# Performance work log

Measured on AMD Instinct MI355X. Metric: run time of the kernel, lower is better.

## Reference

```python
import jax, jax.numpy as jnp
import numpy as np

N_NODES = 100000
N_EDGES = 1600000
IN_DIM = 256
OUT_DIM = 128


def setup_inputs() -> dict:
    key = jax.random.key(0)
    ks = jax.random.split(key, 8)
    x = jax.random.normal(ks[0], (N_NODES, IN_DIM), dtype=jnp.float32)
    # glorot-ish init scaling
    W = jax.random.normal(ks[1], (IN_DIM, OUT_DIM), dtype=jnp.float32) * (6.0 / (IN_DIM + OUT_DIM)) ** 0.5
    fsW = jax.random.normal(ks[2], (IN_DIM, OUT_DIM), dtype=jnp.float32) * (6.0 / (IN_DIM + OUT_DIM)) ** 0.5
    f_weights = jax.random.normal(ks[3], (2 * OUT_DIM, 1), dtype=jnp.float32) * (6.0 / (2 * OUT_DIM + 1)) ** 0.5
    f_bias = jnp.zeros((1,), dtype=jnp.float32)
    # degrees in [1, 64], strictly positive so pow(deg, -p) is finite
    dia_adj = jax.random.uniform(ks[4], (N_NODES,), dtype=jnp.float32) * 63.0 + 1.0
    row = jax.random.randint(ks[5], (N_EDGES,), 0, N_NODES, dtype=jnp.int32)
    col = jax.random.randint(ks[6], (N_EDGES,), 0, N_NODES, dtype=jnp.int32)
    return {"x": x, "W": W, "fsW": fsW, "f_weights": f_weights,
            "f_bias": f_bias, "dia_adj": dia_adj, "row": row, "col": col}


def reference(x, W, fsW, f_weights, f_bias, dia_adj, row, col):
    # pre_sup = x @ weights_, fpre_sup = x @ fs_weights  (dropout=0, dense inputs)
    pre_sup = x @ W                 # [N, out]
    fpre_sup = x @ fsW              # [N, out]
    d = W.shape[1]
    # concat([vi, vj]) @ f_weights == vi @ f_weights[:d] + vj @ f_weights[d:]
    wi, wj = f_weights[:d], f_weights[d:]
    score = jax.nn.sigmoid(fpre_sup[row] @ wi + fpre_sup[col] @ wj + f_bias)  # [E, 1]
    # degree-power normalization: (deg_i * deg_j) ** (-sigmoid_score)
    deg_vivj = (dia_adj[row] * dia_adj[col])[:, None]                         # [E, 1]
    vals = jnp.power(deg_vivj, -score)[:, 0]                                  # [E]
    # sparse matmul: out[r] += vals_e * pre_sup[c] for each edge e=(r,c)
    msg = vals[:, None] * pre_sup[col]                                        # [E, out]
    out = jax.ops.segment_sum(msg, row, num_segments=x.shape[0])              # [N, out]
    return jax.nn.relu(out)
```

## Files before the change

kernel.cpp:

```cpp
#include <hip/hip_runtime.h>

#define N_NODES 100000
#define N_EDGES 1600000
#define IN_DIM 256
#define OUT_DIM 128
#define BROWS 100
#define NBK 1000
#define PBLK 128
#define EPB 12500

typedef __attribute__((ext_vector_type(4))) float f32x4;
typedef __attribute__((ext_vector_type(8))) short s16x8;

__device__ inline unsigned short f2bf(float f) {
    union { float f; unsigned int u; } a; a.f = f;
    unsigned int r = a.u + 0x7fffu + ((a.u >> 16) & 1u);
    return (unsigned short)(r >> 16);
}
__device__ inline float bf2f(unsigned short h) {
    union { unsigned int u; float f; } a; a.u = ((unsigned int)h) << 16;
    return a.f;
}

__global__ __launch_bounds__(256) void kprep(
        const float* __restrict__ fsW, const float* __restrict__ fw,
        const float* __restrict__ W, const int* __restrict__ row,
        float* __restrict__ u, float* __restrict__ v,
        unsigned short* __restrict__ wt, int* __restrict__ hist_t) {
    __shared__ int h[NBK];
    __shared__ float wi[128], wj[128];
    const int t = threadIdx.x, blk = blockIdx.x;
    if (blk < PBLK) {
        wt[blk * 256 + t] = f2bf(W[(size_t)t * 128 + blk]);
        for (int b = t; b < NBK; b += 256) h[b] = 0;
        __syncthreads();
        const int e0 = blk * EPB;
        for (int i = t; i < EPB; i += 256)
            atomicAdd(&h[row[e0 + i] / BROWS], 1);
        __syncthreads();
        for (int b = t; b < NBK; b += 256)
            hist_t[b * PBLK + blk] = h[b];
    } else {
        if (t < 128) wi[t] = fw[t]; else wj[t - 128] = fw[t];
        __syncthreads();
        const float* rowp = fsW + (size_t)t * OUT_DIM;
        float su = 0.f, sv = 0.f;
        for (int d = 0; d < 128; d += 4) {
            float4 a = *(const float4*)(rowp + d);
            su += a.x * wi[d] + a.y * wi[d + 1] + a.z * wi[d + 2] + a.w * wi[d + 3];
            sv += a.x * wj[d] + a.y * wj[d + 1] + a.z * wj[d + 2] + a.w * wj[d + 3];
        }
        u[t] = su; v[t] = sv;
    }
}

__global__ __launch_bounds__(256) void gemm_mfma(
        const float* __restrict__ x, const unsigned short* __restrict__ wt,
        const float* __restrict__ u, const float* __restrict__ v,
        unsigned short* __restrict__ psb, float* __restrict__ si, float* __restrict__ sj) {
    __shared__ unsigned short xa[64 * 136];

    const int t = threadIdx.x;
    const int wave = t >> 6, lane = t & 63;
    const int l15 = lane & 15, lhi = lane >> 4;
    const int row = t >> 2, quad = t & 3;
    const int brow = blockIdx.x * 64;
    const int gnode = brow + row;
    const bool fullblk = (brow + 64 <= N_NODES);
    const bool valid = gnode < N_NODES;

    f32x4 acc[4][2];
#pragma unroll
    for (int mi = 0; mi < 4; ++mi)
#pragma unroll
        for (int ni = 0; ni < 2; ++ni) acc[mi][ni] = (f32x4){0.f, 0.f, 0.f, 0.f};
    float su = 0.f, sv = 0.f;

#pragma unroll
    for (int ph = 0; ph < 2; ++ph) {
        const float* xp = x + (size_t)gnode * IN_DIM + ph * 128 + quad * 32;
        const float* up = u + ph * 128 + quad * 32;
        const float* vp = v + ph * 128 + quad * 32;
        if (fullblk) {
#pragma unroll
            for (int cc = 0; cc < 4; ++cc) {
                float4 a0 = ((const float4*)xp)[cc * 2];
                float4 a1 = ((const float4*)xp)[cc * 2 + 1];
                float4 u0 = ((const float4*)up)[cc * 2], u1 = ((const float4*)up)[cc * 2 + 1];
                float4 v0 = ((const float4*)vp)[cc * 2], v1 = ((const float4*)vp)[cc * 2 + 1];
                su = fmaf(a0.x, u0.x, su); su = fmaf(a0.y, u0.y, su);
                su = fmaf(a0.z, u0.z, su); su = fmaf(a0.w, u0.w, su);
                su = fmaf(a1.x, u1.x, su); su = fmaf(a1.y, u1.y, su);
                su = fmaf(a1.z, u1.z, su); su = fmaf(a1.w, u1.w, su);
                sv = fmaf(a0.x, v0.x, sv); sv = fmaf(a0.y, v0.y, sv);
                sv = fmaf(a0.z, v0.z, sv); sv = fmaf(a0.w, v0.w, sv);
                sv = fmaf(a1.x, v1.x, sv); sv = fmaf(a1.y, v1.y, sv);
                sv = fmaf(a1.z, v1.z, sv); sv = fmaf(a1.w, v1.w, sv);
                union { unsigned short h[8]; uint4 q; } pk;
                pk.h[0] = f2bf(a0.x); pk.h[1] = f2bf(a0.y); pk.h[2] = f2bf(a0.z); pk.h[3] = f2bf(a0.w);
                pk.h[4] = f2bf(a1.x); pk.h[5] = f2bf(a1.y); pk.h[6] = f2bf(a1.z); pk.h[7] = f2bf(a1.w);
                *(uint4*)&xa[row * 136 + quad * 32 + cc * 8] = pk.q;
            }
        } else {
#pragma unroll
            for (int cc = 0; cc < 4; ++cc) {
                float4 a0 = make_float4(0.f, 0.f, 0.f, 0.f), a1 = a0;
                if (valid) {
                    a0 = ((const float4*)xp)[cc * 2];
                    a1 = ((const float4*)xp)[cc * 2 + 1];
                    float4 u0 = ((const float4*)up)[cc * 2], u1 = ((const float4*)up)[cc * 2 + 1];
                    float4 v0 = ((const float4*)vp)[cc * 2], v1 = ((const float4*)vp)[cc * 2 + 1];
                    su = fmaf(a0.x, u0.x, su); su = fmaf(a0.y, u0.y, su);
                    su = fmaf(a0.z, u0.z, su); su = fmaf(a0.w, u0.w, su);
                    su = fmaf(a1.x, u1.x, su); su = fmaf(a1.y, u1.y, su);
                    su = fmaf(a1.z, u1.z, su); su = fmaf(a1.w, u1.w, su);
                    sv = fmaf(a0.x, v0.x, sv); sv = fmaf(a0.y, v0.y, sv);
                    sv = fmaf(a0.z, v0.z, sv); sv = fmaf(a0.w, v0.w, sv);
                    sv = fmaf(a1.x, v1.x, sv); sv = fmaf(a1.y, v1.y, sv);
                    sv = fmaf(a1.z, v1.z, sv); sv = fmaf(a1.w, v1.w, sv);
                }
                union { unsigned short h[8]; uint4 q; } pk;
                pk.h[0] = f2bf(a0.x); pk.h[1] = f2bf(a0.y); pk.h[2] = f2bf(a0.z); pk.h[3] = f2bf(a0.w);
                pk.h[4] = f2bf(a1.x); pk.h[5] = f2bf(a1.y); pk.h[6] = f2bf(a1.z); pk.h[7] = f2bf(a1.w);
                *(uint4*)&xa[row * 136 + quad * 32 + cc * 8] = pk.q;
            }
        }
        __syncthreads();

        {
            const unsigned short* wb0 = wt + (size_t)(wave * 32 + l15) * IN_DIM + ph * 128 + lhi * 8;
            s16x8 bfr[4][2];
#pragma unroll
            for (int ks = 0; ks < 4; ++ks) {
                bfr[ks][0] = *(const s16x8*)(wb0 + ks * 32);
                bfr[ks][1] = *(const s16x8*)(wb0 + (size_t)16 * IN_DIM + ks * 32);
            }
#pragma unroll
            for (int ks = 0; ks < 4; ++ks) {
                const int k0 = ks * 32 + lhi * 8;
                s16x8 afr[4];
#pragma unroll
                for (int mi = 0; mi < 4; ++mi)
                    afr[mi] = *(const s16x8*)&xa[(mi * 16 + l15) * 136 + k0];
#pragma unroll
                for (int mi = 0; mi < 4; ++mi)
#pragma unroll
                    for (int ni = 0; ni < 2; ++ni)
                        acc[mi][ni] = __builtin_amdgcn_mfma_f32_16x16x32_bf16(
                            afr[mi], bfr[ks][ni], acc[mi][ni], 0, 0, 0);
            }
        }
        __syncthreads();
    }

    su += __shfl_xor(su, 1); su += __shfl_xor(su, 2);
    sv += __shfl_xor(sv, 1); sv += __shfl_xor(sv, 2);
    if (quad == 0 && valid) { si[gnode] = su; sj[gnode] = sv; }

    unsigned short* cl = xa;
#pragma unroll
    for (int mi = 0; mi < 4; ++mi)
#pragma unroll
        for (int ni = 0; ni < 2; ++ni) {
            const int colb = wave * 32 + ni * 16 + l15;
#pragma unroll
            for (int j = 0; j < 4; ++j)
                cl[(mi * 16 + lhi * 4 + j) * 128 + colb] = f2bf(acc[mi][ni][j]);
        }
    __syncthreads();
    {
        const int rl = t >> 2;
        const int cb = (t & 3) * 32;
        if (brow + rl < N_NODES) {
            const uint4* src = (const uint4*)&cl[rl * 128 + cb];
            uint4* dst = (uint4*)&psb[(size_t)(brow + rl) * OUT_DIM + cb];
            dst[0] = src[0]; dst[1] = src[1]; dst[2] = src[2]; dst[3] = src[3];
        }
    }
}

__global__ __launch_bounds__(1024) void kbscan(const int* __restrict__ hist_t,
                                               int* __restrict__ bpre) {
    __shared__ int s[1024];
    const int t = threadIdx.x;
    int v = 0;
    if (t < NBK) {
        const int* hp = hist_t + t * PBLK;
        for (int k = 0; k < PBLK; ++k) v += hp[k];
    }
    s[t] = v;
    __syncthreads();
    for (int off = 1; off < 1024; off <<= 1) {
        int nv = (t >= off) ? s[t - off] : 0;
        __syncthreads();
        s[t] += nv;
        __syncthreads();
    }
    if (t < NBK) bpre[t] = s[t] - v;
    if (t == 1023) bpre[NBK] = s[1023];
}

__global__ __launch_bounds__(128) void koff(const int* __restrict__ hist_t,
                                            const int* __restrict__ bpre,
                                            int* __restrict__ off) {
    const int b = blockIdx.x, t = threadIdx.x;
    const int lane = t & 63, w = t >> 6;
    int v = hist_t[b * PBLK + t];
    int s = v;
#pragma unroll
    for (int o = 1; o < 64; o <<= 1) { int tt = __shfl_up(s, o); if (lane >= o) s += tt; }
    __shared__ int ws2[2];
    if (lane == 63) ws2[w] = s;
    __syncthreads();
    int base = (w == 1) ? ws2[0] : 0;
    off[b * PBLK + t] = bpre[b] + base + (s - v);
}

__global__ __launch_bounds__(256) void kpart1(const int* __restrict__ row,
                                              const int* __restrict__ col,
                                              const int* __restrict__ off,
                                              unsigned int* __restrict__ part) {
    __shared__ int cur[NBK];
    const int t = threadIdx.x, blk = blockIdx.x;
    for (int b = t; b < NBK; b += 256) cur[b] = off[b * PBLK + blk];
    __syncthreads();
    const int e0 = blk * EPB;
    for (int i = t; i < EPB; i += 256) {
        int r = row[e0 + i], c = col[e0 + i];
        int b = r / BROWS;
        int rl = r - b * BROWS;
        int pos = atomicAdd(&cur[b], 1);
        part[pos] = ((unsigned)rl << 17) | (unsigned)c;
    }
}

__global__ __launch_bounds__(256) void kpart2(const unsigned int* __restrict__ part,
                                              const int* __restrict__ bpre,
                                              const float* __restrict__ si,
                                              const float* __restrict__ sj,
                                              const float* __restrict__ dia,
                                              const float* __restrict__ fb,
                                              int2* __restrict__ epack,
                                              int* __restrict__ offs,
                                              int* __restrict__ deg) {
    __shared__ int cnt[BROWS];
    __shared__ int cur[BROWS];
    __shared__ float sil[BROWS], dial[BROWS];
    __shared__ int wtot[4];
    const int b = blockIdx.x, t = threadIdx.x;
    const int rbase = b * BROWS;
    if (t < BROWS) {
        cnt[t] = 0;
        sil[t] = si[rbase + t];
        dial[t] = dia[rbase + t];
    }
    __syncthreads();
    const int bstart = bpre[b], bend = bpre[b + 1];
    for (int e = bstart + t; e < bend; e += 256)
        atomicAdd(&cnt[part[e] >> 17], 1);
    __syncthreads();
    {
        int vv = (t < BROWS) ? cnt[t] : 0;
        int lane = t & 63, w = t >> 6;
        int s = vv;
#pragma unroll
        for (int o = 1; o < 64; o <<= 1) { int tt = __shfl_up(s, o); if (lane >= o) s += tt; }
        if (lane == 63) wtot[w] = s;
        __syncthreads();
        int base = 0;
        for (int k = 0; k < w; ++k) base += wtot[k];
        int excl = base + s - vv;
        if (t < BROWS) {
            cur[t] = bstart + excl;
            offs[rbase + t] = bstart + excl;
            deg[rbase + t] = vv;
        }
    }
    __syncthreads();
    const float fbv = fb[0];
    for (int e = bstart + t; e < bend; e += 256) {
        unsigned pk = part[e];
        int rl = (int)(pk >> 17);
        int c = (int)(pk & 0x1FFFFu);
        float tval = sil[rl] + sj[c] + fbv;
        float sg = 1.f / (1.f + expf(-tval));
        float l2 = log2f(dial[rl] * dia[c]);
        float val = exp2f(-sg * l2);
        int pos = atomicAdd(&cur[rl], 1);
        epack[pos] = make_int2(c, __float_as_int(val));
    }
}

__global__ __launch_bounds__(256) void kgather(
        const int* __restrict__ offs, const int* __restrict__ deg,
        const int2* __restrict__ epack,
        const unsigned short* __restrict__ psb, float* __restrict__ out) {
    int lane = threadIdx.x & 31;
    int node = blockIdx.x * 8 + (threadIdx.x >> 5);
    if (node >= N_NODES) return;
    int start = offs[node], d = deg[node];
    const int2* ep = epack + start;
    float a0 = 0.f, a1 = 0.f, a2 = 0.f, a3 = 0.f;
    int k = 0;
    for (; k + 4 <= d; k += 4) {
        int2 e0 = ep[k], e1 = ep[k + 1], e2 = ep[k + 2], e3 = ep[k + 3];
        ushort4 p0 = *(const ushort4*)&psb[(size_t)e0.x * OUT_DIM + lane * 4];
        ushort4 p1 = *(const ushort4*)&psb[(size_t)e1.x * OUT_DIM + lane * 4];
        ushort4 p2 = *(const ushort4*)&psb[(size_t)e2.x * OUT_DIM + lane * 4];
        ushort4 p3 = *(const ushort4*)&psb[(size_t)e3.x * OUT_DIM + lane * 4];
        float v0 = __int_as_float(e0.y), v1 = __int_as_float(e1.y);
        float v2 = __int_as_float(e2.y), v3 = __int_as_float(e3.y);
        a0 = fmaf(v0, bf2f(p0.x), a0); a1 = fmaf(v0, bf2f(p0.y), a1);
        a2 = fmaf(v0, bf2f(p0.z), a2); a3 = fmaf(v0, bf2f(p0.w), a3);
        a0 = fmaf(v1, bf2f(p1.x), a0); a1 = fmaf(v1, bf2f(p1.y), a1);
        a2 = fmaf(v1, bf2f(p1.z), a2); a3 = fmaf(v1, bf2f(p1.w), a3);
        a0 = fmaf(v2, bf2f(p2.x), a0); a1 = fmaf(v2, bf2f(p2.y), a1);
        a2 = fmaf(v2, bf2f(p2.z), a2); a3 = fmaf(v2, bf2f(p2.w), a3);
        a0 = fmaf(v3, bf2f(p3.x), a0); a1 = fmaf(v3, bf2f(p3.y), a1);
        a2 = fmaf(v3, bf2f(p3.z), a2); a3 = fmaf(v3, bf2f(p3.w), a3);
    }
    for (; k < d; ++k) {
        int2 e0 = ep[k];
        float v0 = __int_as_float(e0.y);
        ushort4 p0 = *(const ushort4*)&psb[(size_t)e0.x * OUT_DIM + lane * 4];
        a0 = fmaf(v0, bf2f(p0.x), a0);
        a1 = fmaf(v0, bf2f(p0.y), a1);
        a2 = fmaf(v0, bf2f(p0.z), a2);
        a3 = fmaf(v0, bf2f(p0.w), a3);
    }
    float4 o;
    o.x = fmaxf(a0, 0.f); o.y = fmaxf(a1, 0.f);
    o.z = fmaxf(a2, 0.f); o.w = fmaxf(a3, 0.f);
    *(float4*)&out[(size_t)node * OUT_DIM + lane * 4] = o;
}

extern "C" void kernel_launch(void* const* d_in, const int* in_sizes, int n_in,
                              void* d_out, int out_size, void* d_ws, size_t ws_size,
                              hipStream_t stream) {
    const float* x   = (const float*)d_in[0];
    const float* W   = (const float*)d_in[1];
    const float* fsW = (const float*)d_in[2];
    const float* fw  = (const float*)d_in[3];
    const float* fb  = (const float*)d_in[4];
    const float* dia = (const float*)d_in[5];
    const int*   row = (const int*)d_in[6];
    const int*   col = (const int*)d_in[7];
    float* out = (float*)d_out;

    char* p = (char*)d_ws;
    auto alloc = [&](size_t bytes) -> char* {
        char* r = p; p += (bytes + 255) & ~(size_t)255; return r;
    };
    float* u      = (float*)alloc(256 * 4);
    float* v      = (float*)alloc(256 * 4);
    unsigned short* wtb = (unsigned short*)alloc((size_t)128 * 256 * 2);
    float* si     = (float*)alloc((size_t)N_NODES * 4);
    float* sj     = (float*)alloc((size_t)N_NODES * 4);
    int*   deg    = (int*)alloc((size_t)N_NODES * 4);
    int*   offs   = (int*)alloc((size_t)N_NODES * 4);
    unsigned short* psb = (unsigned short*)alloc((size_t)N_NODES * OUT_DIM * 2);
    int*   hist_t = (int*)alloc((size_t)NBK * PBLK * 4);
    int*   bpre   = (int*)alloc((size_t)(NBK + 1) * 4);
    int*   off    = (int*)alloc((size_t)NBK * PBLK * 4);
    unsigned int* part = (unsigned int*)alloc((size_t)N_EDGES * 4);
    int2*  epack  = (int2*)alloc((size_t)N_EDGES * 8);

    kprep<<<PBLK + 1, 256, 0, stream>>>(fsW, fw, W, row, u, v, wtb, hist_t);
    gemm_mfma<<<(N_NODES + 63) / 64, 256, 0, stream>>>(x, wtb, u, v, psb, si, sj);
    kbscan<<<1, 1024, 0, stream>>>(hist_t, bpre);
    koff<<<NBK, PBLK, 0, stream>>>(hist_t, bpre, off);
    kpart1<<<PBLK, 256, 0, stream>>>(row, col, off, part);
    kpart2<<<NBK, 256, 0, stream>>>(part, bpre, si, sj, dia, fb, epack, offs, deg);
    kgather<<<N_NODES / 8, 256, 0, stream>>>(offs, deg, epack, psb, out);
}
```

Measured before the change: 207.2 us.

## Prefetch x chunks across four GEMM phases, vectorize bscan, unroll gather by eight

The GEMM kernel now splits K into four 64-wide phases. It keeps the next x chunk in registers, loading it while the current phase's MFMAs run, and swaps __syncthreads for raw s_barrier with an explicit lgkmcnt wait. This aims to overlap global loads with compute and shrinks the LDS tile stride. Separately, the block scan sums histograms with int4 loads, and the gather loop is unrolled to eight edges to put more independent loads in flight, at the cost of more registers.

```diff
diff --git a/kernel.cpp b/kernel.cpp
--- a/kernel.cpp
+++ b/kernel.cpp
@@ -66,7 +66,6 @@
     const int row = t >> 2, quad = t & 3;
     const int brow = blockIdx.x * 64;
     const int gnode = brow + row;
-    const bool fullblk = (brow + 64 <= N_NODES);
     const bool valid = gnode < N_NODES;
 
     f32x4 acc[4][2];
@@ -76,72 +75,73 @@
         for (int ni = 0; ni < 2; ++ni) acc[mi][ni] = (f32x4){0.f, 0.f, 0.f, 0.f};
     float su = 0.f, sv = 0.f;
 
-#pragma unroll
-    for (int ph = 0; ph < 2; ++ph) {
-        const float* xp = x + (size_t)gnode * IN_DIM + ph * 128 + quad * 32;
-        const float* up = u + ph * 128 + quad * 32;
-        const float* vp = v + ph * 128 + quad * 32;
-        if (fullblk) {
-#pragma unroll
-            for (int cc = 0; cc < 4; ++cc) {
-                float4 a0 = ((const float4*)xp)[cc * 2];
-                float4 a1 = ((const float4*)xp)[cc * 2 + 1];
-                float4 u0 = ((const float4*)up)[cc * 2], u1 = ((const float4*)up)[cc * 2 + 1];
-                float4 v0 = ((const float4*)vp)[cc * 2], v1 = ((const float4*)vp)[cc * 2 + 1];
-                su = fmaf(a0.x, u0.x, su); su = fmaf(a0.y, u0.y, su);
-                su = fmaf(a0.z, u0.z, su); su = fmaf(a0.w, u0.w, su);
-                su = fmaf(a1.x, u1.x, su); su = fmaf(a1.y, u1.y, su);
-                su = fmaf(a1.z, u1.z, su); su = fmaf(a1.w, u1.w, su);
-                sv = fmaf(a0.x, v0.x, sv); sv = fmaf(a0.y, v0.y, sv);
-                sv = fmaf(a0.z, v0.z, sv); sv = fmaf(a0.w, v0.w, sv);
-                sv = fmaf(a1.x, v1.x, sv); sv = fmaf(a1.y, v1.y, sv);
-                sv = fmaf(a1.z, v1.z, sv); sv = fmaf(a1.w, v1.w, sv);
-                union { unsigned short h[8]; uint4 q; } pk;
-                pk.h[0] = f2bf(a0.x); pk.h[1] = f2bf(a0.y); pk.h[2] = f2bf(a0.z); pk.h[3] = f2bf(a0.w);
-                pk.h[4] = f2bf(a1.x); pk.h[5] = f2bf(a1.y); pk.h[6] = f2bf(a1.z); pk.h[7] = f2bf(a1.w);
-                *(uint4*)&xa[row * 136 + quad * 32 + cc * 8] = pk.q;
+    const float* xp = x + (size_t)gnode * IN_DIM + quad * 16;
+    float4 xr[4];
+#pragma unroll
+    for (int i = 0; i < 4; ++i) xr[i] = make_float4(0.f, 0.f, 0.f, 0.f);
+    if (valid) {
+#pragma unroll
+        for (int i = 0; i < 4; ++i) xr[i] = ((const float4*)xp)[i];
+    }
+
+#pragma unroll
+    for (int ph = 0; ph < 4; ++ph) {
+        {
+            const float* up = u + ph * 64 + quad * 16;
+            const float* vp = v + ph * 64 + quad * 16;
+            float4 uu0 = ((const float4*)up)[0], uu1 = ((const float4*)up)[1];
+            float4 uu2 = ((const float4*)up)[2], uu3 = ((const float4*)up)[3];
+            float4 vv0 = ((const float4*)vp)[0], vv1 = ((const float4*)vp)[1];
+            float4 vv2 = ((const float4*)vp)[2], vv3 = ((const float4*)vp)[3];
+            su = fmaf(xr[0].x, uu0.x, su); su = fmaf(xr[0].y, uu0.y, su);
+            su = fmaf(xr[0].z, uu0.z, su); su = fmaf(xr[0].w, uu0.w, su);
+            su = fmaf(xr[1].x, uu1.x, su); su = fmaf(xr[1].y, uu1.y, su);
+            su = fmaf(xr[1].z, uu1.z, su); su = fmaf(xr[1].w, uu1.w, su);
+            su = fmaf(xr[2].x, uu2.x, su); su = fmaf(xr[2].y, uu2.y, su);
+            su = fmaf(xr[2].z, uu2.z, su); su = fmaf(xr[2].w, uu2.w, su);
+            su = fmaf(xr[3].x, uu3.x, su); su = fmaf(xr[3].y, uu3.y, su);
+            su = fmaf(xr[3].z, uu3.z, su); su = fmaf(xr[3].w, uu3.w, su);
+            sv = fmaf(xr[0].x, vv0.x, sv); sv = fmaf(xr[0].y, vv0.y, sv);
+            sv = fmaf(xr[0].z, vv0.z, sv); sv = fmaf(xr[0].w, vv0.w, sv);
+            sv = fmaf(xr[1].x, vv1.x, sv); sv = fmaf(xr[1].y, vv1.y, sv);
+            sv = fmaf(xr[1].z, vv1.z, sv); sv = fmaf(xr[1].w, vv1.w, sv);
+            sv = fmaf(xr[2].x, vv2.x, sv); sv = fmaf(xr[2].y, vv2.y, sv);
+            sv = fmaf(xr[2].z, vv2.z, sv); sv = fmaf(xr[2].w, vv2.w, sv);
+            sv = fmaf(xr[3].x, vv3.x, sv); sv = fmaf(xr[3].y, vv3.y, sv);
+            sv = fmaf(xr[3].z, vv3.z, sv); sv = fmaf(xr[3].w, vv3.w, sv);
+            union { unsigned short h[16]; uint4 q[2]; } pk;
+#pragma unroll
+            for (int i = 0; i < 4; ++i) {
+                pk.h[i * 4 + 0] = f2bf(xr[i].x); pk.h[i * 4 + 1] = f2bf(xr[i].y);
+                pk.h[i * 4 + 2] = f2bf(xr[i].z); pk.h[i * 4 + 3] = f2bf(xr[i].w);
             }
-        } else {
-#pragma unroll
-            for (int cc = 0; cc < 4; ++cc) {
-                float4 a0 = make_float4(0.f, 0.f, 0.f, 0.f), a1 = a0;
-                if (valid) {
-                    a0 = ((const float4*)xp)[cc * 2];
-                    a1 = ((const float4*)xp)[cc * 2 + 1];
-                    float4 u0 = ((const float4*)up)[cc * 2], u1 = ((const float4*)up)[cc * 2 + 1];
-                    float4 v0 = ((const float4*)vp)[cc * 2], v1 = ((const float4*)vp)[cc * 2 + 1];
-                    su = fmaf(a0.x, u0.x, su); su = fmaf(a0.y, u0.y, su);
-                    su = fmaf(a0.z, u0.z, su); su = fmaf(a0.w, u0.w, su);
-                    su = fmaf(a1.x, u1.x, su); su = fmaf(a1.y, u1.y, su);
-                    su = fmaf(a1.z, u1.z, su); su = fmaf(a1.w, u1.w, su);
-                    sv = fmaf(a0.x, v0.x, sv); sv = fmaf(a0.y, v0.y, sv);
-                    sv = fmaf(a0.z, v0.z, sv); sv = fmaf(a0.w, v0.w, sv);
-                    sv = fmaf(a1.x, v1.x, sv); sv = fmaf(a1.y, v1.y, sv);
-                    sv = fmaf(a1.z, v1.z, sv); sv = fmaf(a1.w, v1.w, sv);
-                }
-                union { unsigned short h[8]; uint4 q; } pk;
-                pk.h[0] = f2bf(a0.x); pk.h[1] = f2bf(a0.y); pk.h[2] = f2bf(a0.z); pk.h[3] = f2bf(a0.w);
-                pk.h[4] = f2bf(a1.x); pk.h[5] = f2bf(a1.y); pk.h[6] = f2bf(a1.z); pk.h[7] = f2bf(a1.w);
-                *(uint4*)&xa[row * 136 + quad * 32 + cc * 8] = pk.q;
+            *(uint4*)&xa[row * 72 + quad * 16]     = pk.q[0];
+            *(uint4*)&xa[row * 72 + quad * 16 + 8] = pk.q[1];
+        }
+        if (ph < 3) {
+            const float* xpn = xp + (ph + 1) * 64;
+            if (valid) {
+#pragma unroll
+                for (int i = 0; i < 4; ++i) xr[i] = ((const float4*)xpn)[i];
             }
         }
-        __syncthreads();
-
+        asm volatile("s_waitcnt lgkmcnt(0)" ::: "memory");
+        __builtin_amdgcn_s_barrier();
         {
-            const unsigned short* wb0 = wt + (size_t)(wave * 32 + l15) * IN_DIM + ph * 128 + lhi * 8;
-            s16x8 bfr[4][2];
-#pragma unroll
-            for (int ks = 0; ks < 4; ++ks) {
+            const unsigned short* wb0 = wt + (size_t)(wave * 32 + l15) * IN_DIM + ph * 64 + lhi * 8;
+            s16x8 bfr[2][2];
+#pragma unroll
+            for (int ks = 0; ks < 2; ++ks) {
                 bfr[ks][0] = *(const s16x8*)(wb0 + ks * 32);
                 bfr[ks][1] = *(const s16x8*)(wb0 + (size_t)16 * IN_DIM + ks * 32);
             }
 #pragma unroll
-            for (int ks = 0; ks < 4; ++ks) {
+            for (int ks = 0; ks < 2; ++ks) {
                 const int k0 = ks * 32 + lhi * 8;
                 s16x8 afr[4];
 #pragma unroll
                 for (int mi = 0; mi < 4; ++mi)
-                    afr[mi] = *(const s16x8*)&xa[(mi * 16 + l15) * 136 + k0];
+                    afr[mi] = *(const s16x8*)&xa[(mi * 16 + l15) * 72 + k0];
 #pragma unroll
                 for (int mi = 0; mi < 4; ++mi)
 #pragma unroll
@@ -150,7 +150,7 @@
                             afr[mi], bfr[ks][ni], acc[mi][ni], 0, 0, 0);
             }
         }
-        __syncthreads();
+        __builtin_amdgcn_s_barrier();
     }
 
     su += __shfl_xor(su, 1); su += __shfl_xor(su, 2);
@@ -185,8 +185,12 @@
     const int t = threadIdx.x;
     int v = 0;
     if (t < NBK) {
-        const int* hp = hist_t + t * PBLK;
-        for (int k = 0; k < PBLK; ++k) v += hp[k];
+        const int4* hp = (const int4*)(hist_t + t * PBLK);
+#pragma unroll 4
+        for (int k = 0; k < PBLK / 4; ++k) {
+            int4 a = hp[k];
+            v += a.x + a.y + a.z + a.w;
+        }
     }
     s[t] = v;
     __syncthreads();
@@ -302,14 +306,21 @@
     const int2* ep = epack + start;
     float a0 = 0.f, a1 = 0.f, a2 = 0.f, a3 = 0.f;
     int k = 0;
-    for (; k + 4 <= d; k += 4) {
-        int2 e0 = ep[k], e1 = ep[k + 1], e2 = ep[k + 2], e3 = ep[k + 3];
+    for (; k + 8 <= d; k += 8) {
+        int2 e0 = ep[k],     e1 = ep[k + 1], e2 = ep[k + 2], e3 = ep[k + 3];
+        int2 e4 = ep[k + 4], e5 = ep[k + 5], e6 = ep[k + 6], e7 = ep[k + 7];
         ushort4 p0 = *(const ushort4*)&psb[(size_t)e0.x * OUT_DIM + lane * 4];
         ushort4 p1 = *(const ushort4*)&psb[(size_t)e1.x * OUT_DIM + lane * 4];
         ushort4 p2 = *(const ushort4*)&psb[(size_t)e2.x * OUT_DIM + lane * 4];
         ushort4 p3 = *(const ushort4*)&psb[(size_t)e3.x * OUT_DIM + lane * 4];
+        ushort4 p4 = *(const ushort4*)&psb[(size_t)e4.x * OUT_DIM + lane * 4];
+        ushort4 p5 = *(const ushort4*)&psb[(size_t)e5.x * OUT_DIM + lane * 4];
+        ushort4 p6 = *(const ushort4*)&psb[(size_t)e6.x * OUT_DIM + lane * 4];
+        ushort4 p7 = *(const ushort4*)&psb[(size_t)e7.x * OUT_DIM + lane * 4];
         float v0 = __int_as_float(e0.y), v1 = __int_as_float(e1.y);
         float v2 = __int_as_float(e2.y), v3 = __int_as_float(e3.y);
+        float v4 = __int_as_float(e4.y), v5 = __int_as_float(e5.y);
+        float v6 = __int_as_float(e6.y), v7 = __int_as_float(e7.y);
         a0 = fmaf(v0, bf2f(p0.x), a0); a1 = fmaf(v0, bf2f(p0.y), a1);
         a2 = fmaf(v0, bf2f(p0.z), a2); a3 = fmaf(v0, bf2f(p0.w), a3);
         a0 = fmaf(v1, bf2f(p1.x), a0); a1 = fmaf(v1, bf2f(p1.y), a1);
@@ -318,6 +329,14 @@
         a2 = fmaf(v2, bf2f(p2.z), a2); a3 = fmaf(v2, bf2f(p2.w), a3);
         a0 = fmaf(v3, bf2f(p3.x), a0); a1 = fmaf(v3, bf2f(p3.y), a1);
         a2 = fmaf(v3, bf2f(p3.z), a2); a3 = fmaf(v3, bf2f(p3.w), a3);
+        a0 = fmaf(v4, bf2f(p4.x), a0); a1 = fmaf(v4, bf2f(p4.y), a1);
+        a2 = fmaf(v4, bf2f(p4.z), a2); a3 = fmaf(v4, bf2f(p4.w), a3);
+        a0 = fmaf(v5, bf2f(p5.x), a0); a1 = fmaf(v5, bf2f(p5.y), a1);
+        a2 = fmaf(v5, bf2f(p5.z), a2); a3 = fmaf(v5, bf2f(p5.w), a3);
+        a0 = fmaf(v6, bf2f(p6.x), a0); a1 = fmaf(v6, bf2f(p6.y), a1);
+        a2 = fmaf(v6, bf2f(p6.z), a2); a3 = fmaf(v6, bf2f(p6.w), a3);
+        a0 = fmaf(v7, bf2f(p7.x), a0); a1 = fmaf(v7, bf2f(p7.y), a1);
+        a2 = fmaf(v7, bf2f(p7.z), a2); a3 = fmaf(v7, bf2f(p7.w), a3);
     }
     for (; k < d; ++k) {
         int2 e0 = ep[k];
```

New measurement: 200.9 us. 3.0% less time.
